# Kernel tuning notes

Hardware: AMD Instinct MI355X
Metric: run time of the kernel (lower is better)

Reference implementation:

```python
import jax, jax.numpy as jnp
import numpy as np

EPS = 1e-12  # F.normalize default eps


def setup_inputs() -> dict:
    key = jax.random.key(0)
    k1, k2, k3, k4 = jax.random.split(key, 4)
    b, c, h, w = 4, 64, 256, 256
    n_class, n = 19, 20
    nc1 = n_class + 1
    content = jax.random.normal(k1, (b, c, h, w), dtype=jnp.float32)
    seg = jax.random.randint(k2, (b, h, w), 0, n_class, dtype=jnp.int32)
    # xavier-normal-ish init for memory params
    key_mem = jax.random.normal(k3, (nc1, c, n), dtype=jnp.float32) * np.sqrt(2.0 / (c + n))
    val_mem = jax.random.normal(k4, (nc1, n, c), dtype=jnp.float32) * np.sqrt(2.0 / (n + c))
    return {"content": content, "seg": seg, "key_mem": key_mem, "val_mem": val_mem}


def reference(content, seg, key_mem, val_mem):
    # content: [b,c,h,w]; seg: [b,h,w] int; key_mem: [K,c,n]; val_mem: [K,n,c], K=n_class+1
    b, c, h, w = content.shape
    K, _, n = key_mem.shape
    p = h * w
    # one-hot class routing (seg shifted by +1 as in original)
    onehot = jax.nn.one_hot(seg.reshape(b, p) + 1, K, dtype=content.dtype)  # [b,p,K]
    # L2-normalize content rows (masked rows in the original are either this
    # normalized vector, for the matching class, or exactly zero)
    cn = content.transpose(0, 2, 3, 1).reshape(b, p, c)
    cn = cn / jnp.maximum(jnp.linalg.norm(cn, axis=-1, keepdims=True), EPS)
    # L2-normalize keys over channel dim (dim=1 of [K,c,n])
    kn = key_mem / jnp.maximum(jnp.linalg.norm(key_mem, axis=1, keepdims=True), EPS)
    # scores for the matching class; non-matching rows are zero -> softmax = uniform 1/n
    scores = jnp.einsum('bpc,kcn->bkpn', cn, kn)         # [b,K,p,n]
    attn = jax.nn.softmax(scores, axis=-1)
    mask = onehot.transpose(0, 2, 1)[..., None]           # [b,K,p,1]
    weight = jnp.where(mask > 0, attn, 1.0 / n)           # [b,K,p,n]
    # bmm with values, then sum over class dim (fused into the einsum)
    out = jnp.einsum('bkpn,knc->bpc', weight, val_mem)    # [b,p,c]
    return out.reshape(b, h, w, c).transpose(0, 3, 1, 2)  # [b,c,h,w]
```

## Files before the change

### kernel.cpp

```cpp
#include <hip/hip_runtime.h>

typedef _Float16 h2 __attribute__((ext_vector_type(2)));
typedef _Float16 h8 __attribute__((ext_vector_type(8)));
typedef float f4 __attribute__((ext_vector_type(4)));
typedef unsigned int uint32;

#define NVAL 20
#define CDIM 64
#define HW   65536
#define NPIX (4*HW)

#define BLK   512
#define NWAVE (BLK/64)
#define MAXTILES 28
#define MAXSLOT  (MAXTILES*64)

#define KN_OFF      0
#define KN_KSTRIDE  2560
#define VAL_OFF     (20*KN_KSTRIDE)
#define VAL_KSTRIDE 4096
#define VAL_CSTRIDE 64

#define ROW_STRIDE 144
#define ROWS_BYTES (BLK*ROW_STRIDE)
#define INV_OFF   ROWS_BYTES
#define PERM_OFF  (INV_OFF + BLK*4)
#define TCLS_OFF  (PERM_OFF + MAXSLOT*2)
#define CNT_OFF   (TCLS_OFF + MAXTILES*4)
#define BASE_OFF  (CNT_OFF + 24*4)
#define NT_OFF    (BASE_OFF + 24*4)
#define LDS_TOTAL (NT_OFF + 16)

static __device__ __forceinline__ h2 bch2(uint32 u) { return __builtin_bit_cast(h2, u); }
static __device__ __forceinline__ uint32 bcu(h2 v) { return __builtin_bit_cast(uint32, v); }
static __device__ __forceinline__ h8 bch8(uint4 u) { return __builtin_bit_cast(h8, u); }
static __device__ __forceinline__ h2 pkrtz(float a, float b) {
    return __builtin_bit_cast(h2, __builtin_amdgcn_cvt_pkrtz(a, b));
}

__global__ void prep_kernel(const float* __restrict__ key,
                            const float* __restrict__ val,
                            unsigned char* __restrict__ ws) {
    int i = blockIdx.x * 256 + threadIdx.x;
    if (i < 20*CDIM) {
        int k = i >> 6, c = i & 63;
        const float* vb = val + k*NVAL*CDIM + c;
        float v[NVAL];
        float s = 0.f;
        #pragma unroll
        for (int j = 0; j < NVAL; j++) { v[j] = vb[j*CDIM]; s += v[j]; }
        float t = 0.f;
        for (int kk = 0; kk < 20; kk++) {
            const float* vb2 = val + kk*NVAL*CDIM + c;
            #pragma unroll
            for (int j = 0; j < NVAL; j++) t += vb2[j*CDIM];
        }
        float rest = (t - s) * (1.0f/NVAL);
        uint32* row = (uint32*)(ws + VAL_OFF + (size_t)k*VAL_KSTRIDE + c*VAL_CSTRIDE);
        #pragma unroll
        for (int jp = 0; jp < 10; jp++) row[jp] = bcu(pkrtz(v[2*jp], v[2*jp+1]));
        row[10] = bcu(pkrtz(rest, 0.f));
        #pragma unroll
        for (int jp = 11; jp < 16; jp++) row[jp] = 0u;
    } else if (i < 20*CDIM + 20*NVAL) {
        int idx = i - 20*CDIM;
        int k = idx / NVAL, j = idx % NVAL;
        const float* kb = key + k*CDIM*NVAL + j;
        float x[CDIM];
        float ssq = 0.f;
        #pragma unroll
        for (int c = 0; c < CDIM; c++) { x[c] = kb[c*NVAL]; ssq = fmaf(x[c], x[c], ssq); }
        float inv = 1.0f / fmaxf(sqrtf(ssq), 1e-12f);
        uint32* row = (uint32*)(ws + KN_OFF + (size_t)k*KN_KSTRIDE + j*128);
        #pragma unroll
        for (int cp = 0; cp < 32; cp++) row[cp] = bcu(pkrtz(x[2*cp]*inv, x[2*cp+1]*inv));
    }
}

__global__ __launch_bounds__(BLK, 4) void main_kernel(
        const float* __restrict__ content, const int* __restrict__ seg,
        const unsigned char* __restrict__ tabs, float* __restrict__ out) {
    extern __shared__ unsigned char lds[];
    float* invA = (float*)(lds + INV_OFF);
    unsigned short* perm = (unsigned short*)(lds + PERM_OFF);
    int* tcls = (int*)(lds + TCLS_OFF);
    int* cnt  = (int*)(lds + CNT_OFF);
    int* base = (int*)(lds + BASE_OFF);
    int* ntp  = (int*)(lds + NT_OFF);

    const int tid  = threadIdx.x;
    const int gp0  = blockIdx.x * BLK;
    const int b    = gp0 >> 16;
    const int pim0 = gp0 & (HW - 1);

    if (tid < 24) cnt[tid] = 0;
    for (int i = tid; i < MAXSLOT; i += BLK) perm[i] = 0xFFFFu;
    __syncthreads();

    const int cls = seg[gp0 + tid] + 1;
    const int myrank = atomicAdd(&cnt[cls], 1);

    {
        const float* cptr = content + (size_t)b * CDIM * HW + pim0 + tid;
        uint2* myrow = (uint2*)(lds + tid * ROW_STRIDE);
        float ssq = 0.f;
        #pragma unroll
        for (int q = 0; q < 16; q++) {
            float f0 = cptr[(size_t)(4*q+0) * HW];
            float f1 = cptr[(size_t)(4*q+1) * HW];
            float f2 = cptr[(size_t)(4*q+2) * HW];
            float f3 = cptr[(size_t)(4*q+3) * HW];
            ssq = fmaf(f0,f0,ssq); ssq = fmaf(f1,f1,ssq);
            ssq = fmaf(f2,f2,ssq); ssq = fmaf(f3,f3,ssq);
            uint2 o; o.x = bcu(pkrtz(f0,f1)); o.y = bcu(pkrtz(f2,f3));
            myrow[q] = o;
        }
        invA[tid] = 1.0f / fmaxf(sqrtf(ssq), 1e-12f);
    }
    __syncthreads();

    if (tid == 0) {
        int off = 0;
        for (int k = 1; k <= 20; k++) { base[k] = off; off += (cnt[k] + 63) & ~63; }
        *ntp = off >> 6;
    }
    __syncthreads();
    {
        int slot = base[cls] + myrank;
        perm[slot] = (unsigned short)tid;
        tcls[slot >> 6] = cls;
    }
    __syncthreads();

    const int nt   = *ntp;
    const int wave = tid >> 6, lane = tid & 63;
    const int g = lane >> 4, r16 = lane & 15;

    for (int t = wave; t < nt; t += NWAVE) {
        const int u = __builtin_amdgcn_readfirstlane(tcls[t]);

        int rowb0, rowb1, rowb2, rowb3;
        float inv0, inv1, inv2, inv3;
        bool mn0, mn1, mn2, mn3;
        {
            int v0 = perm[t*64 + 0*16 + r16]; mn0 = (v0 != 0xFFFF); int l0 = mn0 ? v0 : 0;
            int v1 = perm[t*64 + 1*16 + r16]; mn1 = (v1 != 0xFFFF); int l1 = mn1 ? v1 : 0;
            int v2 = perm[t*64 + 2*16 + r16]; mn2 = (v2 != 0xFFFF); int l2 = mn2 ? v2 : 0;
            int v3 = perm[t*64 + 3*16 + r16]; mn3 = (v3 != 0xFFFF); int l3 = mn3 ? v3 : 0;
            rowb0 = l0*ROW_STRIDE; rowb1 = l1*ROW_STRIDE;
            rowb2 = l2*ROW_STRIDE; rowb3 = l3*ROW_STRIDE;
            inv0 = invA[l0]; inv1 = invA[l1]; inv2 = invA[l2]; inv3 = invA[l3];
        }
        const int rowb[4] = {rowb0, rowb1, rowb2, rowb3};
        const float invn[4] = {inv0, inv1, inv2, inv3};
        const bool mine[4] = {mn0, mn1, mn2, mn3};

        const unsigned char* knc = tabs + KN_OFF + (size_t)u * KN_KSTRIDE;
        uint4 a_sc[2][2];
        #pragma unroll
        for (int m = 0; m < 2; m++)
            #pragma unroll
            for (int ks = 0; ks < 2; ks++)
                a_sc[m][ks] = *(const uint4*)(knc + (m*16 + r16)*128 + (ks*32 + g*8)*2);
        uint4 b_sc[4][2];
        #pragma unroll
        for (int n = 0; n < 4; n++)
            #pragma unroll
            for (int ks = 0; ks < 2; ks++)
                b_sc[n][ks] = *(const uint4*)(lds + rowb[n] + (ks*32 + g*8)*2);

        f4 sacc[2][4];
        #pragma unroll
        for (int m = 0; m < 2; m++)
            #pragma unroll
            for (int n = 0; n < 4; n++) sacc[m][n] = (f4){0.f,0.f,0.f,0.f};
        #pragma unroll
        for (int ks = 0; ks < 2; ks++)
            #pragma unroll
            for (int m = 0; m < 2; m++)
                #pragma unroll
                for (int n = 0; n < 4; n++)
                    sacc[m][n] = __builtin_amdgcn_mfma_f32_16x16x32_f16(
                        bch8(a_sc[m][ks]), bch8(b_sc[n][ks]), sacc[m][n], 0, 0, 0);

        uint2 w0[4], w1[4];
        #pragma unroll
        for (int n = 0; n < 4; n++) {
            float e0[4], e1[4];
            #pragma unroll
            for (int r = 0; r < 4; r++) e0[r] = __expf(sacc[0][n][r] * invn[n]);
            float arg1 = (g == 0) ? invn[n] : 0.0f;
            #pragma unroll
            for (int r = 0; r < 4; r++) e1[r] = __expf(sacc[1][n][r] * arg1);
            float s = e0[0]+e0[1]+e0[2]+e0[3];
            s += (g == 0) ? (e1[0]+e1[1]+e1[2]+e1[3]) : 0.0f;
            s += __shfl_xor(s, 16, 64);
            s += __shfl_xor(s, 32, 64);
            float wsc = 1.0f / s;
            w0[n].x = bcu(pkrtz(e0[0]*wsc, e0[1]*wsc));
            w0[n].y = bcu(pkrtz(e0[2]*wsc, e0[3]*wsc));
            uint2 t1;
            if (g == 0)      { t1.x = bcu(pkrtz(e1[0]*wsc, e1[1]*wsc));
                               t1.y = bcu(pkrtz(e1[2]*wsc, e1[3]*wsc)); }
            else if (g == 1) { t1.x = 0x00003C00u; t1.y = 0u; }
            else             { t1.x = 0u; t1.y = 0u; }
            w1[n] = t1;
        }
        #pragma unroll
        for (int n = 0; n < 4; n++) {
            if (mine[n]) {
                *(uint2*)(lds + rowb[n] + g*8)      = w0[n];
                *(uint2*)(lds + rowb[n] + 32 + g*8) = w1[n];
            }
        }

        uint4 b_pv[4];
        #pragma unroll
        for (int n = 0; n < 4; n++)
            b_pv[n] = *(const uint4*)(lds + rowb[n] + g*16);
        const unsigned char* vc = tabs + VAL_OFF + (size_t)u * VAL_KSTRIDE;
        #pragma unroll
        for (int m = 0; m < 4; m++) {
            uint4 a = *(const uint4*)(vc + (m*16 + r16)*VAL_CSTRIDE + g*16);
            #pragma unroll
            for (int n = 0; n < 4; n++) {
                f4 o = (f4){0.f,0.f,0.f,0.f};
                o = __builtin_amdgcn_mfma_f32_16x16x32_f16(bch8(a), bch8(b_pv[n]), o, 0, 0, 0);
                uint2 ov; ov.x = bcu(pkrtz(o[0], o[1])); ov.y = bcu(pkrtz(o[2], o[3]));
                if (mine[n])
                    *(uint2*)(lds + rowb[n] + m*32 + g*8) = ov;
            }
        }
    }
    __syncthreads();

    {
        const uint2* r2 = (const uint2*)(lds + tid * ROW_STRIDE);
        float* obase = out + (size_t)b * CDIM * HW + pim0 + tid;
        #pragma unroll
        for (int q = 0; q < 16; q++) {
            uint2 v = r2[q];
            h2 x = bch2(v.x), y = bch2(v.y);
            obase[(size_t)(4*q+0) * HW] = (float)x[0];
            obase[(size_t)(4*q+1) * HW] = (float)x[1];
            obase[(size_t)(4*q+2) * HW] = (float)y[0];
            obase[(size_t)(4*q+3) * HW] = (float)y[1];
        }
    }
}

extern "C" void kernel_launch(void* const* d_in, const int* in_sizes, int n_in,
                              void* d_out, int out_size, void* d_ws, size_t ws_size,
                              hipStream_t stream) {
    const float* content = (const float*)d_in[0];
    const int*   seg     = (const int*)d_in[1];
    const float* key     = (const float*)d_in[2];
    const float* val     = (const float*)d_in[3];
    float* out = (float*)d_out;
    unsigned char* ws = (unsigned char*)d_ws;

    prep_kernel<<<7, 256, 0, stream>>>(key, val, ws);

    (void)hipFuncSetAttribute((const void*)main_kernel,
                              hipFuncAttributeMaxDynamicSharedMemorySize, LDS_TOTAL);
    main_kernel<<<NPIX/BLK, BLK, LDS_TOTAL, stream>>>(content, seg, ws, out);
}
```

Baseline: 42.60 us.

## Pad per-class pixel groups to 16 instead of 64 and allow mixed-class tiles

Pixels in a block are bucketed by class and padded to 16-pixel sub-tiles instead of 64-pixel tiles. Each wave then processes four sub-tiles that may belong to different classes, loading key and value tables per sub-tile. This cuts the padded MFMA work caused by rounding each class count up to 64. In exchange it issues more global table loads, since A-operands are fetched per sub-tile and no longer shared across the tile.

Result: slower. 47.96 us (+12.6%).

```diff
diff --git a/kernel.cpp b/kernel.cpp
--- a/kernel.cpp
+++ b/kernel.cpp
@@ -12,8 +12,8 @@
 
 #define BLK   512
 #define NWAVE (BLK/64)
-#define MAXTILES 28
-#define MAXSLOT  (MAXTILES*64)
+#define MAXSUB  52
+#define MAXSLOT (MAXSUB*16)
 
 #define KN_OFF      0
 #define KN_KSTRIDE  2560
@@ -25,8 +25,8 @@
 #define ROWS_BYTES (BLK*ROW_STRIDE)
 #define INV_OFF   ROWS_BYTES
 #define PERM_OFF  (INV_OFF + BLK*4)
-#define TCLS_OFF  (PERM_OFF + MAXSLOT*2)
-#define CNT_OFF   (TCLS_OFF + MAXTILES*4)
+#define SCLS_OFF  (PERM_OFF + MAXSLOT*2)
+#define CNT_OFF   (SCLS_OFF + MAXSUB*4)
 #define BASE_OFF  (CNT_OFF + 24*4)
 #define NT_OFF    (BASE_OFF + 24*4)
 #define LDS_TOTAL (NT_OFF + 16)
@@ -83,7 +83,7 @@
     extern __shared__ unsigned char lds[];
     float* invA = (float*)(lds + INV_OFF);
     unsigned short* perm = (unsigned short*)(lds + PERM_OFF);
-    int* tcls = (int*)(lds + TCLS_OFF);
+    int* scls = (int*)(lds + SCLS_OFF);
     int* cnt  = (int*)(lds + CNT_OFF);
     int* base = (int*)(lds + BASE_OFF);
     int* ntp  = (int*)(lds + NT_OFF);
@@ -94,6 +94,7 @@
     const int pim0 = gp0 & (HW - 1);
 
     if (tid < 24) cnt[tid] = 0;
+    if (tid < MAXSUB) scls[tid] = 0;
     for (int i = tid; i < MAXSLOT; i += BLK) perm[i] = 0xFFFFu;
     __syncthreads();
 
@@ -121,67 +122,57 @@
 
     if (tid == 0) {
         int off = 0;
-        for (int k = 1; k <= 20; k++) { base[k] = off; off += (cnt[k] + 63) & ~63; }
-        *ntp = off >> 6;
+        for (int k = 1; k <= 20; k++) { base[k] = off; off += (cnt[k] + 15) & ~15; }
+        *ntp = off >> 4;
     }
     __syncthreads();
     {
         int slot = base[cls] + myrank;
         perm[slot] = (unsigned short)tid;
-        tcls[slot >> 6] = cls;
-    }
-    __syncthreads();
-
-    const int nt   = *ntp;
+        scls[slot >> 4] = cls;
+    }
+    __syncthreads();
+
+    const int nsub = *ntp;
+    const int ntw  = (nsub + 3) >> 2;
     const int wave = tid >> 6, lane = tid & 63;
     const int g = lane >> 4, r16 = lane & 15;
 
-    for (int t = wave; t < nt; t += NWAVE) {
-        const int u = __builtin_amdgcn_readfirstlane(tcls[t]);
-
-        int rowb0, rowb1, rowb2, rowb3;
-        float inv0, inv1, inv2, inv3;
-        bool mn0, mn1, mn2, mn3;
-        {
-            int v0 = perm[t*64 + 0*16 + r16]; mn0 = (v0 != 0xFFFF); int l0 = mn0 ? v0 : 0;
-            int v1 = perm[t*64 + 1*16 + r16]; mn1 = (v1 != 0xFFFF); int l1 = mn1 ? v1 : 0;
-            int v2 = perm[t*64 + 2*16 + r16]; mn2 = (v2 != 0xFFFF); int l2 = mn2 ? v2 : 0;
-            int v3 = perm[t*64 + 3*16 + r16]; mn3 = (v3 != 0xFFFF); int l3 = mn3 ? v3 : 0;
-            rowb0 = l0*ROW_STRIDE; rowb1 = l1*ROW_STRIDE;
-            rowb2 = l2*ROW_STRIDE; rowb3 = l3*ROW_STRIDE;
-            inv0 = invA[l0]; inv1 = invA[l1]; inv2 = invA[l2]; inv3 = invA[l3];
-        }
-        const int rowb[4] = {rowb0, rowb1, rowb2, rowb3};
-        const float invn[4] = {inv0, inv1, inv2, inv3};
-        const bool mine[4] = {mn0, mn1, mn2, mn3};
-
-        const unsigned char* knc = tabs + KN_OFF + (size_t)u * KN_KSTRIDE;
-        uint4 a_sc[2][2];
+    for (int it = wave; it < ntw; it += NWAVE) {
+        int uu[4], rowb[4];
+        float invn[4];
+        bool mine[4];
+        #pragma unroll
+        for (int n = 0; n < 4; n++) {
+            int sN = it*4 + n;
+            uu[n] = __builtin_amdgcn_readfirstlane(scls[sN]);
+            int v = perm[sN*16 + r16];
+            mine[n] = (v != 0xFFFF);
+            int l = mine[n] ? v : 0;
+            rowb[n] = l * ROW_STRIDE;
+            invn[n] = invA[l];
+        }
+
+        f4 sacc[2][4];
         #pragma unroll
         for (int m = 0; m < 2; m++)
             #pragma unroll
-            for (int ks = 0; ks < 2; ks++)
-                a_sc[m][ks] = *(const uint4*)(knc + (m*16 + r16)*128 + (ks*32 + g*8)*2);
-        uint4 b_sc[4][2];
-        #pragma unroll
-        for (int n = 0; n < 4; n++)
-            #pragma unroll
-            for (int ks = 0; ks < 2; ks++)
-                b_sc[n][ks] = *(const uint4*)(lds + rowb[n] + (ks*32 + g*8)*2);
-
-        f4 sacc[2][4];
-        #pragma unroll
-        for (int m = 0; m < 2; m++)
-            #pragma unroll
             for (int n = 0; n < 4; n++) sacc[m][n] = (f4){0.f,0.f,0.f,0.f};
         #pragma unroll
-        for (int ks = 0; ks < 2; ks++)
-            #pragma unroll
-            for (int m = 0; m < 2; m++)
-                #pragma unroll
-                for (int n = 0; n < 4; n++)
-                    sacc[m][n] = __builtin_amdgcn_mfma_f32_16x16x32_f16(
-                        bch8(a_sc[m][ks]), bch8(b_sc[n][ks]), sacc[m][n], 0, 0, 0);
+        for (int n = 0; n < 4; n++) {
+            const unsigned char* knc = tabs + KN_OFF + (size_t)uu[n] * KN_KSTRIDE;
+            uint4 b0 = *(const uint4*)(lds + rowb[n] + (g*8)*2);
+            uint4 b1 = *(const uint4*)(lds + rowb[n] + (32 + g*8)*2);
+            #pragma unroll
+            for (int m = 0; m < 2; m++) {
+                uint4 a0 = *(const uint4*)(knc + (m*16 + r16)*128 + (g*8)*2);
+                uint4 a1 = *(const uint4*)(knc + (m*16 + r16)*128 + (32 + g*8)*2);
+                sacc[m][n] = __builtin_amdgcn_mfma_f32_16x16x32_f16(
+                    bch8(a0), bch8(b0), sacc[m][n], 0, 0, 0);
+                sacc[m][n] = __builtin_amdgcn_mfma_f32_16x16x32_f16(
+                    bch8(a1), bch8(b1), sacc[m][n], 0, 0, 0);
+            }
+        }
 
         uint2 w0[4], w1[4];
         #pragma unroll
@@ -218,12 +209,12 @@
         #pragma unroll
         for (int n = 0; n < 4; n++)
             b_pv[n] = *(const uint4*)(lds + rowb[n] + g*16);
-        const unsigned char* vc = tabs + VAL_OFF + (size_t)u * VAL_KSTRIDE;
-        #pragma unroll
-        for (int m = 0; m < 4; m++) {
-            uint4 a = *(const uint4*)(vc + (m*16 + r16)*VAL_CSTRIDE + g*16);
-            #pragma unroll
-            for (int n = 0; n < 4; n++) {
+        #pragma unroll
+        for (int n = 0; n < 4; n++) {
+            const unsigned char* vc = tabs + VAL_OFF + (size_t)uu[n] * VAL_KSTRIDE;
+            #pragma unroll
+            for (int m = 0; m < 4; m++) {
+                uint4 a = *(const uint4*)(vc + (m*16 + r16)*VAL_CSTRIDE + g*16);
                 f4 o = (f4){0.f,0.f,0.f,0.f};
                 o = __builtin_amdgcn_mfma_f32_16x16x32_f16(bch8(a), bch8(b_pv[n]), o, 0, 0, 0);
                 uint2 ov; ov.x = bcu(pkrtz(o[0], o[1])); ov.y = bcu(pkrtz(o[2], o[3]));
```
